# Kernel tuning notes

Measured on AMD Instinct MI355X. Metric: run time of the kernel, lower is better.

The kernel has to match this reference:

```python
import jax, jax.numpy as jnp
import numpy as np

B, CIN, COUT, K, H, W = 16, 256, 256, 3, 64, 64
COND = 512


def setup_inputs() -> dict:
    key = jax.random.key(0)
    ks = jax.random.split(key, 10)
    X = jax.random.normal(ks[0], (B, CIN, H, W), dtype=jnp.float32)
    cond_v = jax.random.normal(ks[1], (B, COND), dtype=jnp.float32)
    # conv weight [O, I, kh, kw]
    conv_w = jax.random.normal(ks[2], (COUT, CIN, K, K), dtype=jnp.float32) / np.sqrt(CIN * K * K)
    w0 = jax.random.normal(ks[3], (COND, COND), dtype=jnp.float32) / np.sqrt(COND)
    b0 = jnp.zeros((COND,), dtype=jnp.float32)
    w1 = jax.random.normal(ks[4], (COND, COND), dtype=jnp.float32) / np.sqrt(COND)
    b1 = jnp.zeros((COND,), dtype=jnp.float32)
    w_out = jax.random.normal(ks[5], (CIN, COND), dtype=jnp.float32) / np.sqrt(COND)
    b_out = jnp.zeros((CIN,), dtype=jnp.float32)
    return {"X": X, "cond_v": cond_v, "conv_w": conv_w,
            "w0": w0, "b0": b0, "w1": w1, "b1": b1,
            "w_out": w_out, "b_out": b_out}


def reference(X, cond_v, conv_w, w0, b0, w1, b1, w_out, b_out):
    # proj_cond MLP: (Linear+SiLU) x depth, final Linear -> in_channels
    h = jax.nn.silu(cond_v @ w0.T + b0)
    h = jax.nn.silu(h @ w1.T + b1)
    scale = h @ w_out.T + b_out + 1.0          # [B, I]
    # modulate: bw[b,o,i,kh,kw] = w[o,i,kh,kw] * scale[b,i]
    bw = conv_w[None] * scale[:, None, :, None, None]
    # demodulate across (i, kh, kw)
    demod = jax.lax.rsqrt(jnp.sum(bw * bw, axis=(2, 3, 4)) + 1e-8)  # [B, O]
    bw = bw * demod[:, :, None, None, None]
    b, o, i, kh, kw = bw.shape
    # per-sample conv via grouped conv: x -> [1, B*I, H, W], w -> [B*O, I, kh, kw]
    x = X.reshape(1, b * i, X.shape[2], X.shape[3])
    w = bw.reshape(b * o, i, kh, kw)
    out = jax.lax.conv_general_dilated(
        x, w, window_strides=(1, 1), padding="SAME",
        feature_group_count=b,
        dimension_numbers=("NCHW", "OIHW", "NCHW"))
    return out.reshape(b, o, out.shape[2], out.shape[3])
```

## Files before the change

kernel.cpp:

```cpp
#include <hip/hip_runtime.h>
#include <hip/hip_bf16.h>
#include <cstdint>

#define NB 16
#define CI 256
#define CO 256
#define HH 64
#define WW 64
#define CC 512
#define HP 66
#define WP 66

typedef short short8 __attribute__((ext_vector_type(8)));
typedef float floatx4 __attribute__((ext_vector_type(4)));
typedef unsigned int uintx4 __attribute__((ext_vector_type(4)));

__device__ __forceinline__ void g2lds16(const void* g, void* l) {
  __builtin_amdgcn_global_load_lds((const __attribute__((address_space(1))) void*)g,
                                   (__attribute__((address_space(3))) void*)l, 16, 0, 0);
}

#define ASM_VMCNT0() do { asm volatile("s_waitcnt vmcnt(0)" ::: "memory"); \
                          __builtin_amdgcn_sched_barrier(0); } while (0)
#define ASM_VMCNT2() do { asm volatile("s_waitcnt vmcnt(2)" ::: "memory"); \
                          __builtin_amdgcn_sched_barrier(0); } while (0)
#define ASM_VMCNT3() do { asm volatile("s_waitcnt vmcnt(3)" ::: "memory"); \
                          __builtin_amdgcn_sched_barrier(0); } while (0)
#define RAW_BAR() do { __builtin_amdgcn_sched_barrier(0);  \
                       __builtin_amdgcn_s_barrier();       \
                       __builtin_amdgcn_sched_barrier(0); } while (0)

template<int KD, int N, bool SILU, bool PLUSONE, int BJ>
__global__ void k_mlp(const float* __restrict__ in, const float* __restrict__ w,
                      const float* __restrict__ bias, float* __restrict__ out) {
  __shared__ float4 sin4[KD / 4];
  const int nb = N / BJ;
  int b = blockIdx.x / nb;
  int j = (blockIdx.x % nb) * BJ + threadIdx.x;
  const float4* in4 = reinterpret_cast<const float4*>(in + (size_t)b * KD);
  for (int k = threadIdx.x; k < KD / 4; k += BJ) sin4[k] = in4[k];
  __syncthreads();
  float acc = bias[j];
  const float4* wr = reinterpret_cast<const float4*>(w + (size_t)j * KD);
#pragma unroll 8
  for (int kk = 0; kk < KD / 4; ++kk) {
    float4 wv = wr[kk];
    float4 sv = sin4[kk];
    acc += wv.x * sv.x + wv.y * sv.y + wv.z * sv.z + wv.w * sv.w;
  }
  if (SILU) acc = acc / (1.0f + __expf(-acc));
  if (PLUSONE) acc += 1.0f;
  out[(size_t)b * N + j] = acc;
}

__global__ void k_repack(const float* __restrict__ cw, __hip_bfloat16* __restrict__ Wt,
                         float* __restrict__ wsq) {
  int gid = blockIdx.x * 256 + threadIdx.x;
  if (gid >= CO * CI) return;
  const float* p = cw + (size_t)gid * 9;
  float s = 0.0f;
#pragma unroll
  for (int t = 0; t < 9; ++t) {
    float v = p[t];
    s += v * v;
    Wt[(size_t)t * CO * CI + gid] = __float2bfloat16(v);
  }
  wsq[gid] = s;
}

__global__ void k_demod(const float* __restrict__ wsq, const float* __restrict__ scale,
                        float* __restrict__ demod) {
  __shared__ float s2[CI];
  int b = blockIdx.x;
  int o = threadIdx.x;
  float sv = scale[b * CI + o];
  s2[o] = sv * sv;
  __syncthreads();
  float acc = 0.0f;
  const float4* wr = reinterpret_cast<const float4*>(wsq + (size_t)o * CI);
  const float4* s4 = reinterpret_cast<const float4*>(s2);
#pragma unroll 8
  for (int i = 0; i < CI / 4; ++i) {
    float4 wv = wr[i];
    float4 sq = s4[i];
    acc += wv.x * sq.x + wv.y * sq.y + wv.z * sq.z + wv.w * sq.w;
  }
  demod[b * CO + o] = rsqrtf(acc + 1e-8f);
}

__global__ void k_scalex(const float* __restrict__ X, const float* __restrict__ scale,
                         __hip_bfloat16* __restrict__ Xs) {
  __shared__ float tile[64][68];
  __shared__ float ssc[64];
  int bid = blockIdx.x;
  int b = bid >> 8;
  int rem = bid & 255;
  int h = rem >> 2;
  int i0 = (rem & 3) * 64;
  int t = threadIdx.x;
  if (t < 64) ssc[t] = scale[b * CI + i0 + t];

  __hip_bfloat16* xs_img = Xs + (size_t)b * HP * WP * CI;
  uintx4 z = {0u, 0u, 0u, 0u};
  if (t < 16) {
    int px = (t >> 3) * 65;
    int sl = t & 7;
    *reinterpret_cast<uintx4*>(xs_img + (((size_t)(h + 1)) * WP + px) * CI + i0 + sl * 8) = z;
  }
  if (h == 0) {
    for (int u = t; u < 66 * 8; u += 256) {
      int px = u >> 3, sl = u & 7;
      *reinterpret_cast<uintx4*>(xs_img + ((size_t)px) * CI + i0 + sl * 8) = z;
    }
  }
  if (h == 63) {
    for (int u = t; u < 66 * 8; u += 256) {
      int px = u >> 3, sl = u & 7;
      *reinterpret_cast<uintx4*>(xs_img + ((size_t)65 * WP + px) * CI + i0 + sl * 8) = z;
    }
  }

  const float* src = X + (((size_t)b * CI + i0) * HH + h) * WW;
  int ii_base = t >> 4;
  int w4 = (t & 15) * 4;
#pragma unroll
  for (int r2 = 0; r2 < 4; ++r2) {
    int ii = r2 * 16 + ii_base;
    int key = ((ii >> 3) & 7) << 2;
    *reinterpret_cast<float4*>(&tile[ii][w4 ^ key]) =
        *reinterpret_cast<const float4*>(src + (size_t)ii * HH * WW + w4);
  }
  __syncthreads();
  int u = t & 7;
  int wl = t >> 3;
  int key = u << 2;
#pragma unroll
  for (int iter = 0; iter < 2; ++iter) {
    int w2 = wl + iter * 32;
    union { unsigned short us[8]; uintx4 v; } pk;
#pragma unroll
    for (int j = 0; j < 8; ++j) {
      int ii = u * 8 + j;
      float v = tile[ii][w2 ^ key] * ssc[ii];
      __hip_bfloat16 hb = __float2bfloat16(v);
      pk.us[j] = *reinterpret_cast<unsigned short*>(&hb);
    }
    *reinterpret_cast<uintx4*>(xs_img + (((size_t)(h + 1)) * WP + (w2 + 1)) * CI + i0 + u * 8) = pk.v;
  }
}

__global__ __launch_bounds__(256, 2)
void k_conv(const __hip_bfloat16* __restrict__ Xs, const __hip_bfloat16* __restrict__ Wt,
            const float* __restrict__ demod, float* __restrict__ out) {
  __shared__ __align__(16) char lds[2 * 28672 + 2 * 8192];
  char* sX0 = lds;
  char* sA0 = lds + 57344;

  int wg = (blockIdx.x & 7) * 64 + (blockIdx.x >> 3);
  int b = wg >> 5;
  int rem = wg & 31;
  int ht = rem >> 1;
  int ob = rem & 1;
  int h0 = ht * 4;
  int o0 = ob * 128;

  int tid = threadIdx.x;
  int wv = tid >> 6;
  int lane = tid & 63;
  int lhi = lane >> 4;
  int llo = lane & 15;
  int wo2 = wv >> 1;
  int wpx = wv & 1;

  floatx4 acc[4][8];
#pragma unroll
  for (int m = 0; m < 4; ++m)
#pragma unroll
    for (int n = 0; n < 8; ++n) acc[m][n] = (floatx4){0.f, 0.f, 0.f, 0.f};

  const __hip_bfloat16* xs_img = Xs + (size_t)b * HP * WP * CI;

  int xoff[7];
#pragma unroll
  for (int s = 0; s < 7; ++s) {
    int j = wv + 4 * s;
    int pr = 16 * j + (lane >> 2);
    int prc = pr > 431 ? 431 : pr;
    int lr = prc / 72;
    int wp = prc - lr * 72;
    if (wp > 65) wp = 65;
    int ksl = (lane & 3) ^ ((pr >> 1) & 3);
    xoff[s] = ((h0 + lr) * WP + wp) * CI + ksl * 8;
  }
  int a_off[2];
#pragma unroll
  for (int jj = 0; jj < 2; ++jj) {
    int ol = 32 * wv + 16 * jj + (lane >> 2);
    int sl = (lane & 3) ^ ((ol >> 1) & 3);
    a_off[jj] = (o0 + ol) * CI + sl * 8;
  }

  int row_a[4], key_a[4];
#pragma unroll
  for (int m = 0; m < 4; ++m) {
    row_a[m] = wo2 * 64 + m * 16 + llo;
    key_a[m] = (row_a[m] >> 1) & 3;
  }

#pragma unroll
  for (int s = 0; s < 7; ++s)
    g2lds16(xs_img + xoff[s], sX0 + (wv + 4 * s) * 1024);
#pragma unroll
  for (int jj = 0; jj < 2; ++jj)
    g2lds16(Wt + a_off[jj], sA0 + (wv * 2 + jj) * 1024);
  ASM_VMCNT0();
  RAW_BAR();

  for (int c = 0; c < 8; ++c) {
    const char* xbuf = sX0 + (c & 1) * 28672;
#pragma unroll
    for (int t = 0; t < 9; ++t) {
      int gt = c * 9 + t;
      bool xiss = (t >= 2) && (c < 7);
      if (xiss) {
        int s = t - 2;
        g2lds16(xs_img + xoff[s] + (c + 1) * 32,
                sX0 + ((c + 1) & 1) * 28672 + (wv + 4 * s) * 1024);
      }
      if (gt < 71) {
        int nt = (t == 8) ? 0 : t + 1;
        int ncc = (t == 8) ? c + 1 : c;
        const __hip_bfloat16* wb = Wt + (size_t)nt * CO * CI + ncc * 32;
        char* ad = sA0 + ((gt + 1) & 1) * 8192;
        g2lds16(wb + a_off[0], ad + (wv * 2 + 0) * 1024);
        g2lds16(wb + a_off[1], ad + (wv * 2 + 1) * 1024);
        if (xiss) { ASM_VMCNT3(); } else { ASM_VMCNT2(); }
      } else {
        ASM_VMCNT0();
      }
      RAW_BAR();

      __builtin_amdgcn_s_setprio(1);
      const char* sA = sA0 + (gt & 1) * 8192;
      int kh = t / 3;
      int kw = t - kh * 3;
      short8 af[4];
#pragma unroll
      for (int m = 0; m < 4; ++m)
        af[m] = *reinterpret_cast<const short8*>(sA + row_a[m] * 64 + ((lhi ^ key_a[m]) << 4));
#pragma unroll
      for (int n = 0; n < 8; ++n) {
        int stripe = wpx * 2 + (n >> 2) + kh;
        int px = (n & 3) * 16 + llo + kw;
        int prl = stripe * 72 + px;
        short8 bq = *reinterpret_cast<const short8*>(
            xbuf + prl * 64 + ((lhi ^ ((prl >> 1) & 3)) << 4));
#pragma unroll
        for (int m = 0; m < 4; ++m)
          acc[m][n] = __builtin_amdgcn_mfma_f32_16x16x32_bf16(af[m], bq, acc[m][n], 0, 0, 0);
      }
      __builtin_amdgcn_s_setprio(0);
      RAW_BAR();
    }
  }

#pragma unroll
  for (int m = 0; m < 4; ++m) {
    int obase_o = o0 + wo2 * 64 + m * 16 + lhi * 4;
    float4 dmv = *reinterpret_cast<const float4*>(demod + (size_t)b * CO + obase_o);
#pragma unroll
    for (int j = 0; j < 4; ++j) {
      int o = obase_o + j;
      float dm = (j == 0) ? dmv.x : (j == 1) ? dmv.y : (j == 2) ? dmv.z : dmv.w;
      float* orow = out + (((size_t)b * CO + o) * HH + h0) * WW;
#pragma unroll
      for (int n = 0; n < 8; ++n) {
        int row = wpx * 2 + (n >> 2);
        int col = (n & 3) * 16 + llo;
        orow[(size_t)row * WW + col] = acc[m][n][j] * dm;
      }
    }
  }
}

extern "C" void kernel_launch(void* const* d_in, const int* in_sizes, int n_in,
                              void* d_out, int out_size, void* d_ws, size_t ws_size,
                              hipStream_t stream) {
  const float* X      = (const float*)d_in[0];
  const float* cond_v = (const float*)d_in[1];
  const float* conv_w = (const float*)d_in[2];
  const float* w0     = (const float*)d_in[3];
  const float* b0     = (const float*)d_in[4];
  const float* w1     = (const float*)d_in[5];
  const float* b1     = (const float*)d_in[6];
  const float* w_out  = (const float*)d_in[7];
  const float* b_out  = (const float*)d_in[8];
  float* out = (float*)d_out;

  char* ws = (char*)d_ws;
  const size_t XS_BYTES  = (size_t)NB * HP * WP * CI * 2;
  const size_t WT_BYTES  = (size_t)9 * CO * CI * 2;
  const size_t WSQ_BYTES = (size_t)CO * CI * 4;
  __hip_bfloat16* Xs = (__hip_bfloat16*)ws;
  __hip_bfloat16* Wt = (__hip_bfloat16*)(ws + XS_BYTES);
  float* wsq   = (float*)(ws + XS_BYTES + WT_BYTES);
  float* h0b   = (float*)(ws + XS_BYTES + WT_BYTES + WSQ_BYTES);
  float* h1b   = h0b + NB * CC;
  float* scale = h1b + NB * CC;
  float* demod = scale + NB * CI;

  k_repack<<<(CO * CI) / 256, 256, 0, stream>>>(conv_w, Wt, wsq);
  k_mlp<CC, CC, true, false, 128><<<NB * (CC / 128), 128, 0, stream>>>(cond_v, w0, b0, h0b);
  k_mlp<CC, CC, true, false, 128><<<NB * (CC / 128), 128, 0, stream>>>(h0b, w1, b1, h1b);
  k_mlp<CC, CI, false, true, 128><<<NB * (CI / 128), 128, 0, stream>>>(h1b, w_out, b_out, scale);
  k_demod<<<NB, CO, 0, stream>>>(wsq, scale, demod);
  k_scalex<<<NB * 64 * 4, 256, 0, stream>>>(X, scale, Xs);
  k_conv<<<NB * 32, 256, 0, stream>>>(Xs, Wt, demod, out);
}
```

Measured before the change: 132.1 us.

## Load conv weights directly to registers and software-pipeline LDS fragment reads

Weight fragments are no longer staged through LDS. Each wave now loads its A fragments straight from global memory into registers one tap ahead. X fragments are read from LDS into double-buffered registers one tap ahead, so MFMAs on the current tap overlap the loads for the next one. The per-tap barriers go away, leaving one vmcnt wait and barrier per channel chunk. The cost is higher register pressure and redundant global weight loads across waves, whose latency is now exposed to the register pipeline rather than hidden by LDS.

```diff
diff --git a/kernel.cpp b/kernel.cpp
--- a/kernel.cpp
+++ b/kernel.cpp
@@ -20,11 +20,8 @@
                                    (__attribute__((address_space(3))) void*)l, 16, 0, 0);
 }
 
-#define ASM_VMCNT0() do { asm volatile("s_waitcnt vmcnt(0)" ::: "memory"); \
-                          __builtin_amdgcn_sched_barrier(0); } while (0)
-#define ASM_VMCNT2() do { asm volatile("s_waitcnt vmcnt(2)" ::: "memory"); \
-                          __builtin_amdgcn_sched_barrier(0); } while (0)
-#define ASM_VMCNT3() do { asm volatile("s_waitcnt vmcnt(3)" ::: "memory"); \
+#define ASM_VMCNT0() do { __builtin_amdgcn_sched_barrier(0);            \
+                          asm volatile("s_waitcnt vmcnt(0)" ::: "memory"); \
                           __builtin_amdgcn_sched_barrier(0); } while (0)
 #define RAW_BAR() do { __builtin_amdgcn_sched_barrier(0);  \
                        __builtin_amdgcn_s_barrier();       \
@@ -152,9 +149,8 @@
 __global__ __launch_bounds__(256, 2)
 void k_conv(const __hip_bfloat16* __restrict__ Xs, const __hip_bfloat16* __restrict__ Wt,
             const float* __restrict__ demod, float* __restrict__ out) {
-  __shared__ __align__(16) char lds[2 * 28672 + 2 * 8192];
+  __shared__ __align__(16) char lds[2 * 28672];
   char* sX0 = lds;
-  char* sA0 = lds + 57344;
 
   int wg = (blockIdx.x & 7) * 64 + (blockIdx.x >> 3);
   int b = wg >> 5;
@@ -192,76 +188,88 @@
     int ksl = (lane & 3) ^ ((pr >> 1) & 3);
     xoff[s] = ((h0 + lr) * WP + wp) * CI + ksl * 8;
   }
-  int a_off[2];
-#pragma unroll
-  for (int jj = 0; jj < 2; ++jj) {
-    int ol = 32 * wv + 16 * jj + (lane >> 2);
-    int sl = (lane & 3) ^ ((ol >> 1) & 3);
-    a_off[jj] = (o0 + ol) * CI + sl * 8;
-  }
-
-  int row_a[4], key_a[4];
-#pragma unroll
-  for (int m = 0; m < 4; ++m) {
-    row_a[m] = wo2 * 64 + m * 16 + llo;
-    key_a[m] = (row_a[m] >> 1) & 3;
-  }
+  int aofs[4];
+#pragma unroll
+  for (int m = 0; m < 4; ++m)
+    aofs[m] = (o0 + wo2 * 64 + m * 16 + llo) * CI + lhi * 8;
+
+  short8 bqA[8], bqB[8];
+  short8 afA[4], afB[4];
+
+  auto tap = [&](short8 (&bqc)[8], short8 (&bqn)[8],
+                 short8 (&afc)[4], short8 (&afn)[4], int c, int t) {
+    if (t <= 6 && c < 7)
+      g2lds16(xs_img + xoff[t] + (c + 1) * 32,
+              sX0 + ((c + 1) & 1) * 28672 + (wv + 4 * t) * 1024);
+    bool last = (c == 7) && (t == 8);
+    if (!last) {
+      int tn = (t == 8) ? 0 : t + 1;
+      int cn = (t == 8) ? c + 1 : c;
+      const __hip_bfloat16* wb = Wt + (size_t)tn * CO * CI + cn * 32;
+#pragma unroll
+      for (int m = 0; m < 4; ++m)
+        afn[m] = *reinterpret_cast<const short8*>(wb + aofs[m]);
+    }
+    if (t < 8) {
+      const char* xbuf = sX0 + (c & 1) * 28672;
+      int kh2 = (t + 1) / 3, kw2 = (t + 1) % 3;
+#pragma unroll
+      for (int n = 0; n < 8; ++n) {
+        int prl = (wpx * 2 + (n >> 2) + kh2) * 72 + (n & 3) * 16 + llo + kw2;
+        bqn[n] = *reinterpret_cast<const short8*>(
+            xbuf + prl * 64 + ((lhi ^ ((prl >> 1) & 3)) << 4));
+      }
+    }
+    __builtin_amdgcn_s_setprio(1);
+#pragma unroll
+    for (int n = 0; n < 8; ++n)
+#pragma unroll
+      for (int m = 0; m < 4; ++m)
+        acc[m][n] = __builtin_amdgcn_mfma_f32_16x16x32_bf16(afc[m], bqc[n], acc[m][n], 0, 0, 0);
+    __builtin_amdgcn_s_setprio(0);
+  };
+
+  auto chunk_end = [&](short8 (&bqn)[8], int c) {
+    if (c >= 7) return;
+    ASM_VMCNT0();
+    RAW_BAR();
+    const char* xb = sX0 + ((c + 1) & 1) * 28672;
+#pragma unroll
+    for (int n = 0; n < 8; ++n) {
+      int prl = (wpx * 2 + (n >> 2)) * 72 + (n & 3) * 16 + llo;
+      bqn[n] = *reinterpret_cast<const short8*>(
+          xb + prl * 64 + ((lhi ^ ((prl >> 1) & 3)) << 4));
+    }
+  };
+
+#define TAPB(c, t, CUR, NXT) tap(bq##CUR, bq##NXT, af##CUR, af##NXT, (c), (t))
+#define CHUNK_EVEN(c) do { \
+    TAPB(c,0,A,B); TAPB(c,1,B,A); TAPB(c,2,A,B); TAPB(c,3,B,A); TAPB(c,4,A,B); \
+    TAPB(c,5,B,A); TAPB(c,6,A,B); TAPB(c,7,B,A); TAPB(c,8,A,B); \
+    chunk_end(bqB, (c)); } while (0)
+#define CHUNK_ODD(c) do { \
+    TAPB(c,0,B,A); TAPB(c,1,A,B); TAPB(c,2,B,A); TAPB(c,3,A,B); TAPB(c,4,B,A); \
+    TAPB(c,5,A,B); TAPB(c,6,B,A); TAPB(c,7,A,B); TAPB(c,8,B,A); \
+    chunk_end(bqA, (c)); } while (0)
 
 #pragma unroll
   for (int s = 0; s < 7; ++s)
     g2lds16(xs_img + xoff[s], sX0 + (wv + 4 * s) * 1024);
 #pragma unroll
-  for (int jj = 0; jj < 2; ++jj)
-    g2lds16(Wt + a_off[jj], sA0 + (wv * 2 + jj) * 1024);
+  for (int m = 0; m < 4; ++m)
+    afA[m] = *reinterpret_cast<const short8*>(Wt + aofs[m]);
   ASM_VMCNT0();
   RAW_BAR();
-
-  for (int c = 0; c < 8; ++c) {
-    const char* xbuf = sX0 + (c & 1) * 28672;
-#pragma unroll
-    for (int t = 0; t < 9; ++t) {
-      int gt = c * 9 + t;
-      bool xiss = (t >= 2) && (c < 7);
-      if (xiss) {
-        int s = t - 2;
-        g2lds16(xs_img + xoff[s] + (c + 1) * 32,
-                sX0 + ((c + 1) & 1) * 28672 + (wv + 4 * s) * 1024);
-      }
-      if (gt < 71) {
-        int nt = (t == 8) ? 0 : t + 1;
-        int ncc = (t == 8) ? c + 1 : c;
-        const __hip_bfloat16* wb = Wt + (size_t)nt * CO * CI + ncc * 32;
-        char* ad = sA0 + ((gt + 1) & 1) * 8192;
-        g2lds16(wb + a_off[0], ad + (wv * 2 + 0) * 1024);
-        g2lds16(wb + a_off[1], ad + (wv * 2 + 1) * 1024);
-        if (xiss) { ASM_VMCNT3(); } else { ASM_VMCNT2(); }
-      } else {
-        ASM_VMCNT0();
-      }
-      RAW_BAR();
-
-      __builtin_amdgcn_s_setprio(1);
-      const char* sA = sA0 + (gt & 1) * 8192;
-      int kh = t / 3;
-      int kw = t - kh * 3;
-      short8 af[4];
-#pragma unroll
-      for (int m = 0; m < 4; ++m)
-        af[m] = *reinterpret_cast<const short8*>(sA + row_a[m] * 64 + ((lhi ^ key_a[m]) << 4));
-#pragma unroll
-      for (int n = 0; n < 8; ++n) {
-        int stripe = wpx * 2 + (n >> 2) + kh;
-        int px = (n & 3) * 16 + llo + kw;
-        int prl = stripe * 72 + px;
-        short8 bq = *reinterpret_cast<const short8*>(
-            xbuf + prl * 64 + ((lhi ^ ((prl >> 1) & 3)) << 4));
-#pragma unroll
-        for (int m = 0; m < 4; ++m)
-          acc[m][n] = __builtin_amdgcn_mfma_f32_16x16x32_bf16(af[m], bq, acc[m][n], 0, 0, 0);
-      }
-      __builtin_amdgcn_s_setprio(0);
-      RAW_BAR();
-    }
+#pragma unroll
+  for (int n = 0; n < 8; ++n) {
+    int prl = (wpx * 2 + (n >> 2)) * 72 + (n & 3) * 16 + llo;
+    bqA[n] = *reinterpret_cast<const short8*>(
+        sX0 + prl * 64 + ((lhi ^ ((prl >> 1) & 3)) << 4));
+  }
+
+  for (int c2 = 0; c2 < 8; c2 += 2) {
+    CHUNK_EVEN(c2);
+    CHUNK_ODD(c2 + 1);
   }
 
 #pragma unroll
```

Result: slower. 276.0 us (+109.0%).

## Fuse conditioning MLP and demod into one kernel; triple-buffer conv weight tiles

Applied to the files above, without the earlier changes.

Merges the three MLP launches and the demod launch into a single 512-thread kernel per batch sample, which removes launch overhead and the intermediate global round trips. In the conv kernel, the weight tile ring goes from two to three LDS buffers, which removes the trailing barrier after each tap's MFMA block. The X tile buffer is trimmed to the 27 rows actually used so the total LDS fits. The tap loop is fully unrolled through a macro, and extra sched barriers are placed before the waitcnts. The fused kernel runs only 16 blocks with serial dependent GEMVs, which may underuse the GPU compared with the earlier split launches.

```diff
diff --git a/kernel.cpp b/kernel.cpp
--- a/kernel.cpp
+++ b/kernel.cpp
@@ -20,38 +20,18 @@
                                    (__attribute__((address_space(3))) void*)l, 16, 0, 0);
 }
 
-#define ASM_VMCNT0() do { asm volatile("s_waitcnt vmcnt(0)" ::: "memory"); \
+#define ASM_VMCNT0() do { __builtin_amdgcn_sched_barrier(0);            \
+                          asm volatile("s_waitcnt vmcnt(0)" ::: "memory"); \
                           __builtin_amdgcn_sched_barrier(0); } while (0)
-#define ASM_VMCNT2() do { asm volatile("s_waitcnt vmcnt(2)" ::: "memory"); \
+#define ASM_VMCNT2() do { __builtin_amdgcn_sched_barrier(0);            \
+                          asm volatile("s_waitcnt vmcnt(2)" ::: "memory"); \
                           __builtin_amdgcn_sched_barrier(0); } while (0)
-#define ASM_VMCNT3() do { asm volatile("s_waitcnt vmcnt(3)" ::: "memory"); \
+#define ASM_VMCNT3() do { __builtin_amdgcn_sched_barrier(0);            \
+                          asm volatile("s_waitcnt vmcnt(3)" ::: "memory"); \
                           __builtin_amdgcn_sched_barrier(0); } while (0)
 #define RAW_BAR() do { __builtin_amdgcn_sched_barrier(0);  \
                        __builtin_amdgcn_s_barrier();       \
                        __builtin_amdgcn_sched_barrier(0); } while (0)
-
-template<int KD, int N, bool SILU, bool PLUSONE, int BJ>
-__global__ void k_mlp(const float* __restrict__ in, const float* __restrict__ w,
-                      const float* __restrict__ bias, float* __restrict__ out) {
-  __shared__ float4 sin4[KD / 4];
-  const int nb = N / BJ;
-  int b = blockIdx.x / nb;
-  int j = (blockIdx.x % nb) * BJ + threadIdx.x;
-  const float4* in4 = reinterpret_cast<const float4*>(in + (size_t)b * KD);
-  for (int k = threadIdx.x; k < KD / 4; k += BJ) sin4[k] = in4[k];
-  __syncthreads();
-  float acc = bias[j];
-  const float4* wr = reinterpret_cast<const float4*>(w + (size_t)j * KD);
-#pragma unroll 8
-  for (int kk = 0; kk < KD / 4; ++kk) {
-    float4 wv = wr[kk];
-    float4 sv = sin4[kk];
-    acc += wv.x * sv.x + wv.y * sv.y + wv.z * sv.z + wv.w * sv.w;
-  }
-  if (SILU) acc = acc / (1.0f + __expf(-acc));
-  if (PLUSONE) acc += 1.0f;
-  out[(size_t)b * N + j] = acc;
-}
 
 __global__ void k_repack(const float* __restrict__ cw, __hip_bfloat16* __restrict__ Wt,
                          float* __restrict__ wsq) {
@@ -68,24 +48,77 @@
   wsq[gid] = s;
 }
 
-__global__ void k_demod(const float* __restrict__ wsq, const float* __restrict__ scale,
-                        float* __restrict__ demod) {
+__global__ __launch_bounds__(512)
+void k_cond(const float* __restrict__ cond_v,
+            const float* __restrict__ w0, const float* __restrict__ b0,
+            const float* __restrict__ w1, const float* __restrict__ b1,
+            const float* __restrict__ w_out, const float* __restrict__ b_out,
+            const float* __restrict__ wsq,
+            float* __restrict__ scale, float* __restrict__ demod) {
+  __shared__ float hA[CC];
+  __shared__ float hB[CC];
   __shared__ float s2[CI];
+  __shared__ float sc_s[CI];
   int b = blockIdx.x;
-  int o = threadIdx.x;
-  float sv = scale[b * CI + o];
-  s2[o] = sv * sv;
-  __syncthreads();
-  float acc = 0.0f;
-  const float4* wr = reinterpret_cast<const float4*>(wsq + (size_t)o * CI);
-  const float4* s4 = reinterpret_cast<const float4*>(s2);
+  int j = threadIdx.x;
+
+  hA[j] = cond_v[(size_t)b * CC + j];
+  __syncthreads();
+
+  {
+    float a = b0[j];
+    const float4* wr = reinterpret_cast<const float4*>(w0 + (size_t)j * CC);
+    const float4* iv = reinterpret_cast<const float4*>(hA);
 #pragma unroll 8
-  for (int i = 0; i < CI / 4; ++i) {
-    float4 wv = wr[i];
-    float4 sq = s4[i];
-    acc += wv.x * sq.x + wv.y * sq.y + wv.z * sq.z + wv.w * sq.w;
-  }
-  demod[b * CO + o] = rsqrtf(acc + 1e-8f);
+    for (int k = 0; k < CC / 4; ++k) {
+      float4 w_ = wr[k], v_ = iv[k];
+      a += w_.x * v_.x + w_.y * v_.y + w_.z * v_.z + w_.w * v_.w;
+    }
+    a = a / (1.0f + __expf(-a));
+    hB[j] = a;
+  }
+  __syncthreads();
+
+  {
+    float a = b1[j];
+    const float4* wr = reinterpret_cast<const float4*>(w1 + (size_t)j * CC);
+    const float4* iv = reinterpret_cast<const float4*>(hB);
+#pragma unroll 8
+    for (int k = 0; k < CC / 4; ++k) {
+      float4 w_ = wr[k], v_ = iv[k];
+      a += w_.x * v_.x + w_.y * v_.y + w_.z * v_.z + w_.w * v_.w;
+    }
+    a = a / (1.0f + __expf(-a));
+    hA[j] = a;
+  }
+  __syncthreads();
+
+  if (j < CI) {
+    float sc = b_out[j] + 1.0f;
+    const float4* wr = reinterpret_cast<const float4*>(w_out + (size_t)j * CC);
+    const float4* iv = reinterpret_cast<const float4*>(hA);
+#pragma unroll 8
+    for (int k = 0; k < CC / 4; ++k) {
+      float4 w_ = wr[k], v_ = iv[k];
+      sc += w_.x * v_.x + w_.y * v_.y + w_.z * v_.z + w_.w * v_.w;
+    }
+    sc_s[j] = sc;
+    s2[j] = sc * sc;
+  }
+  __syncthreads();
+
+  if (j < CI) {
+    float acc = 0.0f;
+    const float4* wq = reinterpret_cast<const float4*>(wsq + (size_t)j * CI);
+    const float4* sv = reinterpret_cast<const float4*>(s2);
+#pragma unroll 8
+    for (int k = 0; k < CI / 4; ++k) {
+      float4 w_ = wq[k], v_ = sv[k];
+      acc += w_.x * v_.x + w_.y * v_.y + w_.z * v_.z + w_.w * v_.w;
+    }
+    demod[(size_t)b * CO + j] = rsqrtf(acc + 1e-8f);
+    scale[(size_t)b * CI + j] = sc_s[j];
+  }
 }
 
 __global__ void k_scalex(const float* __restrict__ X, const float* __restrict__ scale,
@@ -152,9 +185,9 @@
 __global__ __launch_bounds__(256, 2)
 void k_conv(const __hip_bfloat16* __restrict__ Xs, const __hip_bfloat16* __restrict__ Wt,
             const float* __restrict__ demod, float* __restrict__ out) {
-  __shared__ __align__(16) char lds[2 * 28672 + 2 * 8192];
+  __shared__ __align__(16) char lds[2 * 27648 + 3 * 8192];
   char* sX0 = lds;
-  char* sA0 = lds + 57344;
+  char* sA0 = lds + 55296;
 
   int wg = (blockIdx.x & 7) * 64 + (blockIdx.x >> 3);
   int b = wg >> 5;
@@ -199,7 +232,6 @@
     int sl = (lane & 3) ^ ((ol >> 1) & 3);
     a_off[jj] = (o0 + ol) * CI + sl * 8;
   }
-
   int row_a[4], key_a[4];
 #pragma unroll
   for (int m = 0; m < 4; ++m) {
@@ -207,61 +239,66 @@
     key_a[m] = (row_a[m] >> 1) & 3;
   }
 
+#define TAP(c, t, CUR, NXT) do {                                                          \
+    bool xi_ = false;                                                                     \
+    if ((t) >= 2 && (t) <= 7 && (c) < 7) {                                                \
+      g2lds16(xs_img + xoff[(t) - 2] + ((c) + 1) * 32,                                    \
+              sX0 + (((c) + 1) & 1) * 27648 + (wv + 4 * ((t) - 2)) * 1024);               \
+      xi_ = true;                                                                         \
+    }                                                                                     \
+    if ((t) == 8 && (c) < 7 && wv < 3) {                                                  \
+      g2lds16(xs_img + xoff[6] + ((c) + 1) * 32,                                          \
+              sX0 + (((c) + 1) & 1) * 27648 + (wv + 24) * 1024);                          \
+      xi_ = true;                                                                         \
+    }                                                                                     \
+    if (!((c) == 7 && (t) == 8)) {                                                        \
+      const __hip_bfloat16* wb_ = Wt +                                                    \
+          (size_t)(((t) == 8) ? 0 : (t) + 1) * CO * CI +                                  \
+          (size_t)(((t) == 8) ? (c) + 1 : (c)) * 32;                                      \
+      g2lds16(wb_ + a_off[0], sA0 + (NXT) * 8192 + (wv * 2 + 0) * 1024);                  \
+      g2lds16(wb_ + a_off[1], sA0 + (NXT) * 8192 + (wv * 2 + 1) * 1024);                  \
+      if (xi_) { ASM_VMCNT3(); } else { ASM_VMCNT2(); }                                   \
+    } else {                                                                              \
+      ASM_VMCNT0();                                                                       \
+    }                                                                                     \
+    RAW_BAR();                                                                            \
+    {                                                                                     \
+      const char* sA_ = sA0 + (CUR) * 8192;                                               \
+      const char* xb_ = sX0 + ((c) & 1) * 27648;                                          \
+      const int kh_ = (t) / 3, kw_ = (t) % 3;                                             \
+      short8 af_[4];                                                                      \
+      _Pragma("unroll")                                                                   \
+      for (int m = 0; m < 4; ++m)                                                         \
+        af_[m] = *reinterpret_cast<const short8*>(                                        \
+            sA_ + row_a[m] * 64 + ((lhi ^ key_a[m]) << 4));                               \
+      __builtin_amdgcn_s_setprio(1);                                                      \
+      _Pragma("unroll")                                                                   \
+      for (int n = 0; n < 8; ++n) {                                                       \
+        int prl = (wpx * 2 + (n >> 2) + kh_) * 72 + (n & 3) * 16 + llo + kw_;             \
+        short8 bq_ = *reinterpret_cast<const short8*>(                                    \
+            xb_ + prl * 64 + ((lhi ^ ((prl >> 1) & 3)) << 4));                            \
+        _Pragma("unroll")                                                                 \
+        for (int m = 0; m < 4; ++m)                                                       \
+          acc[m][n] = __builtin_amdgcn_mfma_f32_16x16x32_bf16(af_[m], bq_,                \
+                                                              acc[m][n], 0, 0, 0);       \
+      }                                                                                   \
+      __builtin_amdgcn_s_setprio(0);                                                      \
+    }                                                                                     \
+  } while (0)
+
 #pragma unroll
   for (int s = 0; s < 7; ++s)
-    g2lds16(xs_img + xoff[s], sX0 + (wv + 4 * s) * 1024);
-#pragma unroll
-  for (int jj = 0; jj < 2; ++jj)
-    g2lds16(Wt + a_off[jj], sA0 + (wv * 2 + jj) * 1024);
-  ASM_VMCNT0();
+    if (wv + 4 * s < 27)
+      g2lds16(xs_img + xoff[s], sX0 + (wv + 4 * s) * 1024);
+  g2lds16(Wt + a_off[0], sA0 + (wv * 2 + 0) * 1024);
+  g2lds16(Wt + a_off[1], sA0 + (wv * 2 + 1) * 1024);
+  ASM_VMCNT2();
   RAW_BAR();
 
   for (int c = 0; c < 8; ++c) {
-    const char* xbuf = sX0 + (c & 1) * 28672;
-#pragma unroll
-    for (int t = 0; t < 9; ++t) {
-      int gt = c * 9 + t;
-      bool xiss = (t >= 2) && (c < 7);
-      if (xiss) {
-        int s = t - 2;
-        g2lds16(xs_img + xoff[s] + (c + 1) * 32,
-                sX0 + ((c + 1) & 1) * 28672 + (wv + 4 * s) * 1024);
-      }
-      if (gt < 71) {
-        int nt = (t == 8) ? 0 : t + 1;
-        int ncc = (t == 8) ? c + 1 : c;
-        const __hip_bfloat16* wb = Wt + (size_t)nt * CO * CI + ncc * 32;
-        char* ad = sA0 + ((gt + 1) & 1) * 8192;
-        g2lds16(wb + a_off[0], ad + (wv * 2 + 0) * 1024);
-        g2lds16(wb + a_off[1], ad + (wv * 2 + 1) * 1024);
-        if (xiss) { ASM_VMCNT3(); } else { ASM_VMCNT2(); }
-      } else {
-        ASM_VMCNT0();
-      }
-      RAW_BAR();
-
-      __builtin_amdgcn_s_setprio(1);
-      const char* sA = sA0 + (gt & 1) * 8192;
-      int kh = t / 3;
-      int kw = t - kh * 3;
-      short8 af[4];
-#pragma unroll
-      for (int m = 0; m < 4; ++m)
-        af[m] = *reinterpret_cast<const short8*>(sA + row_a[m] * 64 + ((lhi ^ key_a[m]) << 4));
-#pragma unroll
-      for (int n = 0; n < 8; ++n) {
-        int stripe = wpx * 2 + (n >> 2) + kh;
-        int px = (n & 3) * 16 + llo + kw;
-        int prl = stripe * 72 + px;
-        short8 bq = *reinterpret_cast<const short8*>(
-            xbuf + prl * 64 + ((lhi ^ ((prl >> 1) & 3)) << 4));
-#pragma unroll
-        for (int m = 0; m < 4; ++m)
-          acc[m][n] = __builtin_amdgcn_mfma_f32_16x16x32_bf16(af[m], bq, acc[m][n], 0, 0, 0);
-      }
-      __builtin_amdgcn_s_setprio(0);
-      RAW_BAR();
-    }
+    TAP(c, 0, 0, 1); TAP(c, 1, 1, 2); TAP(c, 2, 2, 0);
+    TAP(c, 3, 0, 1); TAP(c, 4, 1, 2); TAP(c, 5, 2, 0);
+    TAP(c, 6, 0, 1); TAP(c, 7, 1, 2); TAP(c, 8, 2, 0);
   }
 
 #pragma unroll
@@ -281,6 +318,7 @@
       }
     }
   }
+#undef TAP
 }
 
 extern "C" void kernel_launch(void* const* d_in, const int* in_sizes, int n_in,
@@ -304,16 +342,11 @@
   __hip_bfloat16* Xs = (__hip_bfloat16*)ws;
   __hip_bfloat16* Wt = (__hip_bfloat16*)(ws + XS_BYTES);
   float* wsq   = (float*)(ws + XS_BYTES + WT_BYTES);
-  float* h0b   = (float*)(ws + XS_BYTES + WT_BYTES + WSQ_BYTES);
-  float* h1b   = h0b + NB * CC;
-  float* scale = h1b + NB * CC;
+  float* scale = (float*)(ws + XS_BYTES + WT_BYTES + WSQ_BYTES);
   float* demod = scale + NB * CI;
 
   k_repack<<<(CO * CI) / 256, 256, 0, stream>>>(conv_w, Wt, wsq);
-  k_mlp<CC, CC, true, false, 128><<<NB * (CC / 128), 128, 0, stream>>>(cond_v, w0, b0, h0b);
-  k_mlp<CC, CC, true, false, 128><<<NB * (CC / 128), 128, 0, stream>>>(h0b, w1, b1, h1b);
-  k_mlp<CC, CI, false, true, 128><<<NB * (CI / 128), 128, 0, stream>>>(h1b, w_out, b_out, scale);
-  k_demod<<<NB, CO, 0, stream>>>(wsq, scale, demod);
+  k_cond<<<NB, 512, 0, stream>>>(cond_v, w0, b0, w1, b1, w_out, b_out, wsq, scale, demod);
   k_scalex<<<NB * 64 * 4, 256, 0, stream>>>(X, scale, Xs);
   k_conv<<<NB * 32, 256, 0, stream>>>(Xs, Wt, demod, out);
 }
```

Measured after the change: 325.2 us. 146% more time.

## Fuse conditioning MLP layers and demodulation into one per-sample kernel

Applied to the files above, without the earlier changes.

Replaces the three k_mlp launches and the k_demod launch with a single k_cond kernel: one 512-thread block per sample runs all three linear layers and the demodulation sum, keeping intermediates in shared memory. This removes three kernel launches and the global round trips for the hidden activations. In exchange, only 16 blocks run, each thread reading full weight rows serially, so the MLP gets far less parallelism than the previous 64-block launches.

```diff
diff --git a/kernel.cpp b/kernel.cpp
--- a/kernel.cpp
+++ b/kernel.cpp
@@ -30,29 +30,6 @@
                        __builtin_amdgcn_s_barrier();       \
                        __builtin_amdgcn_sched_barrier(0); } while (0)
 
-template<int KD, int N, bool SILU, bool PLUSONE, int BJ>
-__global__ void k_mlp(const float* __restrict__ in, const float* __restrict__ w,
-                      const float* __restrict__ bias, float* __restrict__ out) {
-  __shared__ float4 sin4[KD / 4];
-  const int nb = N / BJ;
-  int b = blockIdx.x / nb;
-  int j = (blockIdx.x % nb) * BJ + threadIdx.x;
-  const float4* in4 = reinterpret_cast<const float4*>(in + (size_t)b * KD);
-  for (int k = threadIdx.x; k < KD / 4; k += BJ) sin4[k] = in4[k];
-  __syncthreads();
-  float acc = bias[j];
-  const float4* wr = reinterpret_cast<const float4*>(w + (size_t)j * KD);
-#pragma unroll 8
-  for (int kk = 0; kk < KD / 4; ++kk) {
-    float4 wv = wr[kk];
-    float4 sv = sin4[kk];
-    acc += wv.x * sv.x + wv.y * sv.y + wv.z * sv.z + wv.w * sv.w;
-  }
-  if (SILU) acc = acc / (1.0f + __expf(-acc));
-  if (PLUSONE) acc += 1.0f;
-  out[(size_t)b * N + j] = acc;
-}
-
 __global__ void k_repack(const float* __restrict__ cw, __hip_bfloat16* __restrict__ Wt,
                          float* __restrict__ wsq) {
   int gid = blockIdx.x * 256 + threadIdx.x;
@@ -68,24 +45,77 @@
   wsq[gid] = s;
 }
 
-__global__ void k_demod(const float* __restrict__ wsq, const float* __restrict__ scale,
-                        float* __restrict__ demod) {
+__global__ __launch_bounds__(512)
+void k_cond(const float* __restrict__ cond_v,
+            const float* __restrict__ w0, const float* __restrict__ b0,
+            const float* __restrict__ w1, const float* __restrict__ b1,
+            const float* __restrict__ w_out, const float* __restrict__ b_out,
+            const float* __restrict__ wsq,
+            float* __restrict__ scale, float* __restrict__ demod) {
+  __shared__ float hA[CC];
+  __shared__ float hB[CC];
   __shared__ float s2[CI];
+  __shared__ float sc_s[CI];
   int b = blockIdx.x;
-  int o = threadIdx.x;
-  float sv = scale[b * CI + o];
-  s2[o] = sv * sv;
-  __syncthreads();
-  float acc = 0.0f;
-  const float4* wr = reinterpret_cast<const float4*>(wsq + (size_t)o * CI);
-  const float4* s4 = reinterpret_cast<const float4*>(s2);
+  int j = threadIdx.x;
+
+  hA[j] = cond_v[(size_t)b * CC + j];
+  __syncthreads();
+
+  {
+    float a = b0[j];
+    const float4* wr = reinterpret_cast<const float4*>(w0 + (size_t)j * CC);
+    const float4* iv = reinterpret_cast<const float4*>(hA);
 #pragma unroll 8
-  for (int i = 0; i < CI / 4; ++i) {
-    float4 wv = wr[i];
-    float4 sq = s4[i];
-    acc += wv.x * sq.x + wv.y * sq.y + wv.z * sq.z + wv.w * sq.w;
-  }
-  demod[b * CO + o] = rsqrtf(acc + 1e-8f);
+    for (int k = 0; k < CC / 4; ++k) {
+      float4 w_ = wr[k], v_ = iv[k];
+      a += w_.x * v_.x + w_.y * v_.y + w_.z * v_.z + w_.w * v_.w;
+    }
+    a = a / (1.0f + __expf(-a));
+    hB[j] = a;
+  }
+  __syncthreads();
+
+  {
+    float a = b1[j];
+    const float4* wr = reinterpret_cast<const float4*>(w1 + (size_t)j * CC);
+    const float4* iv = reinterpret_cast<const float4*>(hB);
+#pragma unroll 8
+    for (int k = 0; k < CC / 4; ++k) {
+      float4 w_ = wr[k], v_ = iv[k];
+      a += w_.x * v_.x + w_.y * v_.y + w_.z * v_.z + w_.w * v_.w;
+    }
+    a = a / (1.0f + __expf(-a));
+    hA[j] = a;
+  }
+  __syncthreads();
+
+  if (j < CI) {
+    float sc = b_out[j] + 1.0f;
+    const float4* wr = reinterpret_cast<const float4*>(w_out + (size_t)j * CC);
+    const float4* iv = reinterpret_cast<const float4*>(hA);
+#pragma unroll 8
+    for (int k = 0; k < CC / 4; ++k) {
+      float4 w_ = wr[k], v_ = iv[k];
+      sc += w_.x * v_.x + w_.y * v_.y + w_.z * v_.z + w_.w * v_.w;
+    }
+    sc_s[j] = sc;
+    s2[j] = sc * sc;
+  }
+  __syncthreads();
+
+  if (j < CI) {
+    float acc = 0.0f;
+    const float4* wq = reinterpret_cast<const float4*>(wsq + (size_t)j * CI);
+    const float4* sv = reinterpret_cast<const float4*>(s2);
+#pragma unroll 8
+    for (int k = 0; k < CI / 4; ++k) {
+      float4 w_ = wq[k], v_ = sv[k];
+      acc += w_.x * v_.x + w_.y * v_.y + w_.z * v_.z + w_.w * v_.w;
+    }
+    demod[(size_t)b * CO + j] = rsqrtf(acc + 1e-8f);
+    scale[(size_t)b * CI + j] = sc_s[j];
+  }
 }
 
 __global__ void k_scalex(const float* __restrict__ X, const float* __restrict__ scale,
@@ -304,16 +334,11 @@
   __hip_bfloat16* Xs = (__hip_bfloat16*)ws;
   __hip_bfloat16* Wt = (__hip_bfloat16*)(ws + XS_BYTES);
   float* wsq   = (float*)(ws + XS_BYTES + WT_BYTES);
-  float* h0b   = (float*)(ws + XS_BYTES + WT_BYTES + WSQ_BYTES);
-  float* h1b   = h0b + NB * CC;
-  float* scale = h1b + NB * CC;
+  float* scale = (float*)(ws + XS_BYTES + WT_BYTES + WSQ_BYTES);
   float* demod = scale + NB * CI;
 
   k_repack<<<(CO * CI) / 256, 256, 0, stream>>>(conv_w, Wt, wsq);
-  k_mlp<CC, CC, true, false, 128><<<NB * (CC / 128), 128, 0, stream>>>(cond_v, w0, b0, h0b);
-  k_mlp<CC, CC, true, false, 128><<<NB * (CC / 128), 128, 0, stream>>>(h0b, w1, b1, h1b);
-  k_mlp<CC, CI, false, true, 128><<<NB * (CI / 128), 128, 0, stream>>>(h1b, w_out, b_out, scale);
-  k_demod<<<NB, CO, 0, stream>>>(wsq, scale, demod);
+  k_cond<<<NB, 512, 0, stream>>>(cond_v, w0, b0, w1, b1, w_out, b_out, wsq, scale, demod);
   k_scalex<<<NB * 64 * 4, 256, 0, stream>>>(X, scale, Xs);
   k_conv<<<NB * 32, 256, 0, stream>>>(Xs, Wt, demod, out);
 }
```

New measurement: 169.8 us. 28.5% more time.
